# Kernel optimization log

Hardware: AMD Instinct MI355X
Metric: run time of the kernel (lower is better)

## Reference

```python
import jax, jax.numpy as jnp
import numpy as np

D_MODEL = 512
INF = 1e9
TEMP = np.sqrt(D_MODEL).astype(np.float32)


def setup_inputs() -> dict:
    key = jax.random.key(0)
    kq, kk, kv, km = jax.random.split(key, 4)
    B, L, D = 64, 1024, 64  # B = batch*heads
    q = jax.random.normal(kq, (B, L, D), dtype=jnp.float32)
    k = jax.random.normal(kk, (B, L, D), dtype=jnp.float32)
    v = jax.random.normal(kv, (B, L, D), dtype=jnp.float32)
    attn_mask = jax.random.randint(km, (B, L, L), 0, 2).astype(jnp.bool_)
    return {"q": q, "k": k, "v": v, "attn_mask": attn_mask}


def reference(q, k, v, attn_mask):
    # scores: [b, len_q, len_k]
    attn = jnp.einsum('bqd,bkd->bqk', q, k) / TEMP
    attn = jnp.where(attn_mask, -INF, attn)
    attn = jax.nn.softmax(attn, axis=2)
    # dropout p=0.0 -> identity
    out = jnp.einsum('bqk,bkd->bqd', attn, v)
    return out
```

## Files before the change

### kernel.cpp

```cpp
#include <hip/hip_runtime.h>
#include <hip/hip_bf16.h>


typedef __attribute__((ext_vector_type(4))) float f32x4;
typedef __attribute__((ext_vector_type(8))) short bf16x8;
typedef __attribute__((ext_vector_type(4))) short short4v;

constexpr int B_ = 64;
constexpr int L_ = 1024;
constexpr int D_ = 64;
constexpr int QBLK = 64;
constexpr int KV = 64;
constexpr int NKV = L_ / KV;
constexpr int STR = 72;
constexpr int STRB = 72;
constexpr float INV_TEMP = 0.04419417382415922f;
constexpr float NEG = -1e9f;

__device__ inline short f2bf(float f) {
  __hip_bfloat16 h = __float2bfloat16(f);
  short s; __builtin_memcpy(&s, &h, 2);
  return s;
}

__global__ __launch_bounds__(256) void attn_fwd(
    const float* __restrict__ Q, const float* __restrict__ K,
    const float* __restrict__ V, const int* __restrict__ M,
    float* __restrict__ O)
{
  __shared__ short k_lds[KV][STR];
  __shared__ short vt_lds[D_][STR];
  __shared__ short p_lds[4][16][STR];
  __shared__ unsigned char m_lds[QBLK][STRB];

  const int qt   = blockIdx.x;
  const int b    = blockIdx.y;
  const int tid  = threadIdx.x;
  const int w    = tid >> 6;
  const int lane = tid & 63;
  const int g    = lane >> 4;
  const int c    = lane & 15;

  const int q0 = qt * QBLK;

  bf16x8 qf[2];
  {
    const float* qp = Q + ((size_t)b * L_ + q0 + w * 16 + c) * D_ + g * 8;
#pragma unroll
    for (int ks = 0; ks < 2; ++ks) {
      f32x4 x0 = *(const f32x4*)(qp + ks * 32);
      f32x4 x1 = *(const f32x4*)(qp + ks * 32 + 4);
      bf16x8 t;
      t[0] = f2bf(x0[0]); t[1] = f2bf(x0[1]); t[2] = f2bf(x0[2]); t[3] = f2bf(x0[3]);
      t[4] = f2bf(x1[0]); t[5] = f2bf(x1[1]); t[6] = f2bf(x1[2]); t[7] = f2bf(x1[3]);
      qf[ks] = t;
    }
  }

  const float* Kb = K + (size_t)b * L_ * D_;
  const float* Vb = V + (size_t)b * L_ * D_;
  const int*   Mb = M + (size_t)b * L_ * L_ + (size_t)q0 * L_;

  f32x4 kreg[4], vreg[4];
  int4  mreg[4];
  const int vkey4 = (tid & 15) * 4;
  const int vd4   = (tid >> 4) * 4;

  auto stage_load = [&](int t) {
    const float* ksrc = Kb + (size_t)(t * KV) * D_;
    const float* vsrc = Vb + (size_t)(t * KV) * D_;
    const int*   msrc = Mb + t * KV;
#pragma unroll
    for (int i = 0; i < 4; ++i) {
      const int idx = tid + i * 256;
      const int row = idx >> 4;
      const int d4  = (idx & 15) * 4;
      kreg[i] = *(const f32x4*)(ksrc + (size_t)idx * 4);
      mreg[i] = *(const int4*)(msrc + (size_t)row * L_ + d4);
      vreg[i] = *(const f32x4*)(vsrc + (size_t)(vkey4 + i) * D_ + vd4);
    }
  };

  auto stage_write = [&]() {
#pragma unroll
    for (int i = 0; i < 4; ++i) {
      const int idx = tid + i * 256;
      const int row = idx >> 4;
      const int d4  = (idx & 15) * 4;
      f32x4 kx = kreg[i];
      short4v ks4 = { f2bf(kx[0]), f2bf(kx[1]), f2bf(kx[2]), f2bf(kx[3]) };
      *(short4v*)&k_lds[row][d4] = ks4;
      int4 mm = mreg[i];
      unsigned int packed = (unsigned int)(mm.x != 0)
                          | ((unsigned int)(mm.y != 0) << 8)
                          | ((unsigned int)(mm.z != 0) << 16)
                          | ((unsigned int)(mm.w != 0) << 24);
      *(unsigned int*)&m_lds[row][d4] = packed;
      const int jj = (i + (tid >> 4)) & 3;
      short4v vt4 = { f2bf(vreg[0][jj]), f2bf(vreg[1][jj]),
                      f2bf(vreg[2][jj]), f2bf(vreg[3][jj]) };
      *(short4v*)&vt_lds[vd4 + jj][vkey4] = vt4;
    }
  };

  f32x4 acc[4];
#pragma unroll
  for (int i = 0; i < 4; ++i) acc[i] = (f32x4){0.f, 0.f, 0.f, 0.f};
  float m_run = -INFINITY;
  float l_run = 0.f;

  stage_load(0);
  stage_write();
  __syncthreads();

  for (int t = 0; t < NKV; ++t) {
    const bool has_next = (t + 1 < NKV);
    if (has_next) stage_load(t + 1);

    f32x4 sc[4];
#pragma unroll
    for (int f = 0; f < 4; ++f) {
      f32x4 a = (f32x4){0.f, 0.f, 0.f, 0.f};
#pragma unroll
      for (int ks = 0; ks < 2; ++ks) {
        bf16x8 kf = *(const bf16x8*)&k_lds[f * 16 + c][ks * 32 + g * 8];
        a = __builtin_amdgcn_mfma_f32_16x16x32_bf16(kf, qf[ks], a, 0, 0, 0);
      }
      sc[f] = a;
    }

    const unsigned char* mrow = &m_lds[w * 16 + c][0];
#pragma unroll
    for (int f = 0; f < 4; ++f) {
      const unsigned int mm4 = *(const unsigned int*)(mrow + f * 16 + 4 * g);
#pragma unroll
      for (int r = 0; r < 4; ++r) {
        sc[f][r] = ((mm4 >> (8 * r)) & 0xffu) ? NEG : sc[f][r] * INV_TEMP;
      }
    }

    float x = -INFINITY;
#pragma unroll
    for (int f = 0; f < 4; ++f)
#pragma unroll
      for (int r = 0; r < 4; ++r) x = fmaxf(x, sc[f][r]);
    x = fmaxf(x, __shfl_xor(x, 16, 64));
    x = fmaxf(x, __shfl_xor(x, 32, 64));
    const float m_new = fmaxf(m_run, x);
    const float alpha = __expf(m_run - m_new);
    float s = 0.f;
#pragma unroll
    for (int f = 0; f < 4; ++f)
#pragma unroll
      for (int r = 0; r < 4; ++r) {
        sc[f][r] = __expf(sc[f][r] - m_new);
        s += sc[f][r];
      }
    s += __shfl_xor(s, 16, 64);
    s += __shfl_xor(s, 32, 64);
    l_run = l_run * alpha + s;
    m_run = m_new;

    float ar[4];
#pragma unroll
    for (int r = 0; r < 4; ++r)
      ar[r] = __shfl(alpha, (lane & 48) | (g * 4 + r), 64);
#pragma unroll
    for (int fd = 0; fd < 4; ++fd)
#pragma unroll
      for (int r = 0; r < 4; ++r) acc[fd][r] *= ar[r];

#pragma unroll
    for (int f = 0; f < 4; ++f) {
      short4v pk = { f2bf(sc[f][0]), f2bf(sc[f][1]), f2bf(sc[f][2]), f2bf(sc[f][3]) };
      *(short4v*)&p_lds[w][c][f * 16 + 4 * g] = pk;
    }

#pragma unroll
    for (int ks = 0; ks < 2; ++ks) {
      bf16x8 pa = *(const bf16x8*)&p_lds[w][c][ks * 32 + g * 8];
#pragma unroll
      for (int fd = 0; fd < 4; ++fd) {
        bf16x8 vb = *(const bf16x8*)&vt_lds[fd * 16 + c][ks * 32 + g * 8];
        acc[fd] = __builtin_amdgcn_mfma_f32_16x16x32_bf16(pa, vb, acc[fd], 0, 0, 0);
      }
    }

    __syncthreads();
    if (has_next) stage_write();
    __syncthreads();
  }

  const float li = 1.0f / l_run;
  float lr[4];
#pragma unroll
  for (int r = 0; r < 4; ++r)
    lr[r] = __shfl(li, (lane & 48) | (g * 4 + r), 64);
  float* orow = O + ((size_t)b * L_ + q0 + w * 16 + g * 4) * D_;
#pragma unroll
  for (int fd = 0; fd < 4; ++fd)
#pragma unroll
    for (int r = 0; r < 4; ++r)
      orow[(size_t)r * D_ + fd * 16 + c] = acc[fd][r] * lr[r];
}

extern "C" void kernel_launch(void* const* d_in, const int* in_sizes, int n_in,
                              void* d_out, int out_size, void* d_ws, size_t ws_size,
                              hipStream_t stream) {
  const float* q = (const float*)d_in[0];
  const float* k = (const float*)d_in[1];
  const float* v = (const float*)d_in[2];
  const int* m = (const int*)d_in[3];
  float* o = (float*)d_out;
  dim3 grid(L_ / QBLK, B_);
  attn_fwd<<<grid, 256, 0, stream>>>(q, k, v, m, o);
}
```

Before: 108.9 us.

## Double-buffer K/V in LDS and load mask directly into registers

K and V tiles now alternate between two LDS buffers, so the next tile can be written right after the current tile's MMAs and each iteration needs only one barrier instead of two. The mask is no longer staged through LDS. Each lane loads its own mask entries straight from global memory into registers, ping-ponging between two register sets across an unrolled pair of iterations. This removes the mask LDS traffic and one sync per tile, at the cost of more LDS for the K/V buffers, more registers, and less coalesced per-lane mask loads.

New measurement: 100.3 us. 1.09x faster.

```diff
diff --git a/kernel.cpp b/kernel.cpp
--- a/kernel.cpp
+++ b/kernel.cpp
@@ -13,7 +13,6 @@
 constexpr int KV = 64;
 constexpr int NKV = L_ / KV;
 constexpr int STR = 72;
-constexpr int STRB = 72;
 constexpr float INV_TEMP = 0.04419417382415922f;
 constexpr float NEG = -1e9f;
 
@@ -28,20 +27,17 @@
     const float* __restrict__ V, const int* __restrict__ M,
     float* __restrict__ O)
 {
-  __shared__ short k_lds[KV][STR];
-  __shared__ short vt_lds[D_][STR];
+  __shared__ short k_lds[2][KV][STR];
+  __shared__ short vt_lds[2][D_][STR];
   __shared__ short p_lds[4][16][STR];
-  __shared__ unsigned char m_lds[QBLK][STRB];
-
-  const int qt   = blockIdx.x;
-  const int b    = blockIdx.y;
+
   const int tid  = threadIdx.x;
   const int w    = tid >> 6;
   const int lane = tid & 63;
   const int g    = lane >> 4;
   const int c    = lane & 15;
-
-  const int q0 = qt * QBLK;
+  const int b    = blockIdx.y;
+  const int q0   = blockIdx.x * QBLK;
 
   bf16x8 qf[2];
   {
@@ -59,29 +55,27 @@
 
   const float* Kb = K + (size_t)b * L_ * D_;
   const float* Vb = V + (size_t)b * L_ * D_;
-  const int*   Mb = M + (size_t)b * L_ * L_ + (size_t)q0 * L_;
+  const int* mlane = M + (size_t)b * L_ * L_ + (size_t)(q0 + w * 16 + c) * L_ + 4 * g;
 
   f32x4 kreg[4], vreg[4];
-  int4  mreg[4];
+  int4  mA[4], mB[4];
   const int vkey4 = (tid & 15) * 4;
   const int vd4   = (tid >> 4) * 4;
 
-  auto stage_load = [&](int t) {
+  auto load_kv = [&](int t) {
     const float* ksrc = Kb + (size_t)(t * KV) * D_;
     const float* vsrc = Vb + (size_t)(t * KV) * D_;
-    const int*   msrc = Mb + t * KV;
 #pragma unroll
     for (int i = 0; i < 4; ++i) {
-      const int idx = tid + i * 256;
-      const int row = idx >> 4;
-      const int d4  = (idx & 15) * 4;
-      kreg[i] = *(const f32x4*)(ksrc + (size_t)idx * 4);
-      mreg[i] = *(const int4*)(msrc + (size_t)row * L_ + d4);
+      kreg[i] = *(const f32x4*)(ksrc + (size_t)(tid + i * 256) * 4);
       vreg[i] = *(const f32x4*)(vsrc + (size_t)(vkey4 + i) * D_ + vd4);
     }
   };
-
-  auto stage_write = [&]() {
+  auto load_m = [&](int t, int4 (&mr)[4]) {
+#pragma unroll
+    for (int f = 0; f < 4; ++f) mr[f] = *(const int4*)(mlane + t * KV + f * 16);
+  };
+  auto write_kv = [&](int buf) {
 #pragma unroll
     for (int i = 0; i < 4; ++i) {
       const int idx = tid + i * 256;
@@ -89,17 +83,11 @@
       const int d4  = (idx & 15) * 4;
       f32x4 kx = kreg[i];
       short4v ks4 = { f2bf(kx[0]), f2bf(kx[1]), f2bf(kx[2]), f2bf(kx[3]) };
-      *(short4v*)&k_lds[row][d4] = ks4;
-      int4 mm = mreg[i];
-      unsigned int packed = (unsigned int)(mm.x != 0)
-                          | ((unsigned int)(mm.y != 0) << 8)
-                          | ((unsigned int)(mm.z != 0) << 16)
-                          | ((unsigned int)(mm.w != 0) << 24);
-      *(unsigned int*)&m_lds[row][d4] = packed;
+      *(short4v*)&k_lds[buf][row][d4] = ks4;
       const int jj = (i + (tid >> 4)) & 3;
       short4v vt4 = { f2bf(vreg[0][jj]), f2bf(vreg[1][jj]),
                       f2bf(vreg[2][jj]), f2bf(vreg[3][jj]) };
-      *(short4v*)&vt_lds[vd4 + jj][vkey4] = vt4;
+      *(short4v*)&vt_lds[buf][vd4 + jj][vkey4] = vt4;
     }
   };
 
@@ -109,13 +97,14 @@
   float m_run = -INFINITY;
   float l_run = 0.f;
 
-  stage_load(0);
-  stage_write();
+  load_kv(0);
+  load_m(0, mA);
+  write_kv(0);
   __syncthreads();
 
-  for (int t = 0; t < NKV; ++t) {
-    const bool has_next = (t + 1 < NKV);
-    if (has_next) stage_load(t + 1);
+  auto body = [&](int t, bool has_next, int4 (&mc)[4], int4 (&mn)[4]) {
+    const int cur = t & 1;
+    if (has_next) { load_kv(t + 1); load_m(t + 1, mn); }
 
     f32x4 sc[4];
 #pragma unroll
@@ -123,20 +112,19 @@
       f32x4 a = (f32x4){0.f, 0.f, 0.f, 0.f};
 #pragma unroll
       for (int ks = 0; ks < 2; ++ks) {
-        bf16x8 kf = *(const bf16x8*)&k_lds[f * 16 + c][ks * 32 + g * 8];
+        bf16x8 kf = *(const bf16x8*)&k_lds[cur][f * 16 + c][ks * 32 + g * 8];
         a = __builtin_amdgcn_mfma_f32_16x16x32_bf16(kf, qf[ks], a, 0, 0, 0);
       }
       sc[f] = a;
     }
 
-    const unsigned char* mrow = &m_lds[w * 16 + c][0];
 #pragma unroll
     for (int f = 0; f < 4; ++f) {
-      const unsigned int mm4 = *(const unsigned int*)(mrow + f * 16 + 4 * g);
-#pragma unroll
-      for (int r = 0; r < 4; ++r) {
-        sc[f][r] = ((mm4 >> (8 * r)) & 0xffu) ? NEG : sc[f][r] * INV_TEMP;
-      }
+      const int4 mm = mc[f];
+      sc[f][0] = mm.x ? NEG : sc[f][0] * INV_TEMP;
+      sc[f][1] = mm.y ? NEG : sc[f][1] * INV_TEMP;
+      sc[f][2] = mm.z ? NEG : sc[f][2] * INV_TEMP;
+      sc[f][3] = mm.w ? NEG : sc[f][3] * INV_TEMP;
     }
 
     float x = -INFINITY;
@@ -181,14 +169,18 @@
       bf16x8 pa = *(const bf16x8*)&p_lds[w][c][ks * 32 + g * 8];
 #pragma unroll
       for (int fd = 0; fd < 4; ++fd) {
-        bf16x8 vb = *(const bf16x8*)&vt_lds[fd * 16 + c][ks * 32 + g * 8];
+        bf16x8 vb = *(const bf16x8*)&vt_lds[cur][fd * 16 + c][ks * 32 + g * 8];
         acc[fd] = __builtin_amdgcn_mfma_f32_16x16x32_bf16(pa, vb, acc[fd], 0, 0, 0);
       }
     }
 
+    if (has_next) write_kv(cur ^ 1);
     __syncthreads();
-    if (has_next) stage_write();
-    __syncthreads();
+  };
+
+  for (int tt = 0; tt < NKV; tt += 2) {
+    body(tt,     true,          mA, mB);
+    body(tt + 1, tt + 2 < NKV,  mB, mA);
   }
 
   const float li = 1.0f / l_run;
```
